# Kernel optimization log

Hardware: AMD Instinct MI355X
Metric: run time of the kernel (lower is better)

Reference implementation:

```python
import jax, jax.numpy as jnp
import numpy as np

NEG_SLOPE = 0.01  # torch LeakyReLU default
MIN_FREQ = 1.0
MAX_FREQ = 10.0
W = 100
N_HIDDEN = 100
N_OBS = 64

def _leaky(x):
    return jnp.where(x >= 0, x, NEG_SLOPE * x)

def setup_inputs() -> dict:
    key = jax.random.key(0)
    ks = jax.random.split(key, 7)
    # kaiming_uniform-ish init scales (exact init doesn't matter for correctness baseline)
    def unif(k, shape, fan_in):
        bound = np.sqrt(6.0 / fan_in)
        return jax.random.uniform(k, shape, jnp.float32, -bound, bound)
    x = jax.random.normal(ks[0], (65536, N_OBS), jnp.float32)
    W_in = unif(ks[1], (N_OBS, W), N_OBS)
    b_in = jnp.zeros((W,), jnp.float32)
    Ws = unif(ks[2], (N_HIDDEN, W, W), W)
    bs = jnp.zeros((N_HIDDEN, W), jnp.float32)
    W_out = unif(ks[3], (W, 1), W)
    b_out = jnp.zeros((1,), jnp.float32)
    return {"x": x, "W_in": W_in, "b_in": b_in, "Ws": Ws, "bs": bs,
            "W_out": W_out, "b_out": b_out}

def reference(x, W_in, b_in, Ws, bs, W_out, b_out):
    h = _leaky(x @ W_in + b_in)                       # [B, 100]
    def layer(h, wb):
        w, b = wb
        return _leaky(h @ w + b), None
    h, _ = jax.lax.scan(layer, h, (Ws, bs))           # 100 hidden layers
    a = h @ W_out + b_out                             # [B, 1]
    a = jnp.tanh(a)
    return (a + 1.0) / 2.0 * (MAX_FREQ - MIN_FREQ) + MIN_FREQ
```

## Files before the change

### kernel.cpp

```cpp
#include <hip/hip_runtime.h>
#include <cmath>

#define NLAYERS 100
#define DIN     64
#define WDIM    100
#define NPAD    112
#define NT      7
#define ROWS    32
#define PSTR    136
#define PLANE   (16 * PSTR)

typedef _Float16 half8 __attribute__((ext_vector_type(8)));
typedef __fp16   fp16x2 __attribute__((ext_vector_type(2)));
typedef float    f32x4 __attribute__((ext_vector_type(4)));

#define WSH_LAYER_HALVES (NT * 4 * 64 * 8)
#define WSH_HALVES       (NLAYERS * WSH_LAYER_HALVES)
#define W0_HALVES        (NT * 2 * 64 * 8)
#define BPAD_FLOATS      ((NLAYERS + 1) * NPAD)
#define OFF_BPAD_B       ((WSH_HALVES + W0_HALVES) * 2)
#define OFF_WOUT_B       (OFF_BPAD_B + BPAD_FLOATS * 4)
#define TOTAL_PREP       (WSH_HALVES + W0_HALVES + BPAD_FLOATS + NPAD)

__global__ void actor_prep(const float* __restrict__ Win, const float* __restrict__ bin,
                           const float* __restrict__ Ws,  const float* __restrict__ bs,
                           const float* __restrict__ Wout,
                           _Float16* __restrict__ wsh, _Float16* __restrict__ w0sh,
                           float* __restrict__ bpad, float* __restrict__ woutp) {
    int t = blockIdx.x * 256 + threadIdx.x;
    if (t < WSH_HALVES) {
        int j    = t & 7;
        int lane = (t >> 3) & 63;
        int ks   = (t >> 9) & 3;
        int rest = t >> 11;
        int nt   = rest % 7;
        int l    = rest / 7;
        int qq = lane >> 4, ll = lane & 15;
        int k = ks * 32 + qq * 8 + j;
        int n = nt * 16 + ll;
        float v = 0.f;
        if (k < WDIM && n < WDIM)       v = Ws[(l * WDIM + k) * WDIM + n];
        else if (k == 112 && n < WDIM)  v = bs[l * WDIM + n];
        wsh[t] = (_Float16)v;
        return;
    }
    int t2 = t - WSH_HALVES;
    if (t2 < W0_HALVES) {
        int j    = t2 & 7;
        int lane = (t2 >> 3) & 63;
        int ks   = (t2 >> 9) & 1;
        int nt   = t2 >> 10;
        int qq = lane >> 4, ll = lane & 15;
        int k = ks * 32 + qq * 8 + j;
        int n = nt * 16 + ll;
        float v = (k < DIN && n < WDIM) ? Win[k * WDIM + n] : 0.f;
        w0sh[t2] = (_Float16)v;
        return;
    }
    int t3 = t2 - W0_HALVES;
    if (t3 < BPAD_FLOATS) {
        int l = t3 / NPAD, c = t3 % NPAD;
        float v = 0.f;
        if (c < WDIM) v = (l == 0) ? bin[c] : bs[(l - 1) * WDIM + c];
        bpad[t3] = v;
        return;
    }
    int t4 = t3 - BPAD_FLOATS;
    if (t4 < NPAD) woutp[t4] = (t4 < WDIM) ? Wout[t4] : 0.f;
}

__device__ __forceinline__ void split8(const float* __restrict__ p, half8& hi, half8& lo) {
    f32x4 u0 = *(const f32x4*)p;
    f32x4 u1 = *(const f32x4*)(p + 4);
    float v[8] = {u0[0], u0[1], u0[2], u0[3], u1[0], u1[1], u1[2], u1[3]};
#pragma unroll
    for (int e = 0; e < 8; e += 2) {
        fp16x2 h = __builtin_amdgcn_cvt_pkrtz(v[e], v[e + 1]);
        float r0 = v[e]     - (float)h[0];
        float r1 = v[e + 1] - (float)h[1];
        fp16x2 l = __builtin_amdgcn_cvt_pkrtz(r0, r1);
        hi[e] = (_Float16)h[0]; hi[e + 1] = (_Float16)h[1];
        lo[e] = (_Float16)l[0]; lo[e + 1] = (_Float16)l[1];
    }
}

__device__ __forceinline__ void ep_tile(const f32x4 a, _Float16* __restrict__ d) {
    d[0] = (_Float16)fmaxf(a[0], 0.01f * a[0]);
    d[1] = (_Float16)fmaxf(a[1], 0.01f * a[1]);
    d[2] = (_Float16)fmaxf(a[2], 0.01f * a[2]);
    d[3] = (_Float16)fmaxf(a[3], 0.01f * a[3]);
}

__global__ __launch_bounds__(64, 2)
void actor_main(const float* __restrict__ x,
                const _Float16* __restrict__ wsh,
                const _Float16* __restrict__ w0sh,
                const float* __restrict__ bpad,
                const float* __restrict__ woutp,
                const float* __restrict__ bout,
                float* __restrict__ out) {
    __shared__ _Float16 hp[2 * PLANE];
    const int lane = threadIdx.x;
    const int q = lane >> 4, l15 = lane & 15;
    const int rowbase = blockIdx.x * ROWS;

    f32x4 acc0[NT], acc1[NT];
    half8 wb[4][NT];
    const f32x4 zero4 = {0.f, 0.f, 0.f, 0.f};

    {
        if (lane < 32) {
            const int pl = lane >> 4, row = lane & 15;
            const half8 z = {0, 0, 0, 0, 0, 0, 0, 0};
            *(half8*)(hp + pl * PLANE + row * PSTR + 112) = z;
            *(half8*)(hp + pl * PLANE + row * PSTR + 120) = z;
            hp[pl * PLANE + row * PSTR + 112] = (_Float16)1.0f;
        }
    }

#pragma unroll
    for (int ks = 0; ks < 2; ++ks)
#pragma unroll
        for (int nt = 0; nt < NT; ++nt)
            wb[ks][nt] = *(const half8*)(w0sh + ((nt * 2 + ks) * 64 + lane) * 8);
#pragma unroll
    for (int nt = 0; nt < NT; ++nt) {
        f32x4 b = *(const f32x4*)(bpad + nt * 16 + q * 4);
        acc0[nt] = b;
        acc1[nt] = b;
    }
#pragma unroll
    for (int ks = 0; ks < 2; ++ks) {
        half8 xhi, xlo;
        split8(x + (rowbase + l15) * DIN + ks * 32 + q * 8, xhi, xlo);
#pragma unroll
        for (int nt = 0; nt < NT; ++nt) {
            acc0[nt] = __builtin_amdgcn_mfma_f32_16x16x32_f16(wb[ks][nt], xhi, acc0[nt], 0, 0, 0);
            acc0[nt] = __builtin_amdgcn_mfma_f32_16x16x32_f16(wb[ks][nt], xlo, acc0[nt], 0, 0, 0);
        }
    }
#pragma unroll
    for (int ks = 0; ks < 2; ++ks) {
        half8 xhi, xlo;
        split8(x + (rowbase + 16 + l15) * DIN + ks * 32 + q * 8, xhi, xlo);
#pragma unroll
        for (int nt = 0; nt < NT; ++nt) {
            acc1[nt] = __builtin_amdgcn_mfma_f32_16x16x32_f16(wb[ks][nt], xhi, acc1[nt], 0, 0, 0);
            acc1[nt] = __builtin_amdgcn_mfma_f32_16x16x32_f16(wb[ks][nt], xlo, acc1[nt], 0, 0, 0);
        }
    }
#pragma unroll
    for (int ks = 0; ks < 4; ++ks)
#pragma unroll
        for (int nt = 0; nt < NT; ++nt)
            wb[ks][nt] = *(const half8*)(wsh + (ks * 64 + lane) * 8 + nt * 4 * 64 * 8);
#pragma unroll
    for (int nt = 0; nt < NT; ++nt)
        ep_tile(acc0[nt], hp + l15 * PSTR + nt * 16 + q * 4);

#pragma unroll 1
    for (int l = 0; l < NLAYERS; ++l) {
        const _Float16* wn = wsh + (l < NLAYERS - 1 ? l + 1 : l) * WSH_LAYER_HALVES;

        {
            f32x4 p1[NT];
#pragma unroll
            for (int nt = 0; nt < NT; ++nt) { p1[nt] = acc1[nt]; acc0[nt] = zero4; }
            _Float16* d1 = hp + PLANE + l15 * PSTR + q * 4;
#pragma unroll
            for (int ks = 0; ks < 4; ++ks) {
                half8 b0 = *(const half8*)(hp + l15 * PSTR + ks * 32 + q * 8);
#pragma unroll
                for (int nt = 0; nt < NT; ++nt)
                    acc0[nt] = __builtin_amdgcn_mfma_f32_16x16x32_f16(wb[ks][nt], b0, acc0[nt], 0, 0, 0);
                ep_tile(p1[2 * ks], d1 + (2 * ks) * 16);
                if (ks < 3) ep_tile(p1[2 * ks + 1], d1 + (2 * ks + 1) * 16);
            }
        }

        {
            f32x4 p0[NT];
#pragma unroll
            for (int nt = 0; nt < NT; ++nt) { p0[nt] = acc0[nt]; acc1[nt] = zero4; }
            _Float16* d0 = hp + l15 * PSTR + q * 4;
#pragma unroll
            for (int ks = 0; ks < 4; ++ks) {
                half8 b1 = *(const half8*)(hp + PLANE + l15 * PSTR + ks * 32 + q * 8);
#pragma unroll
                for (int nt = 0; nt < NT; ++nt)
                    acc1[nt] = __builtin_amdgcn_mfma_f32_16x16x32_f16(wb[ks][nt], b1, acc1[nt], 0, 0, 0);
#pragma unroll
                for (int nt = 0; nt < NT; ++nt)
                    wb[ks][nt] = *(const half8*)(wn + (ks * 64 + lane) * 8 + nt * 4 * 64 * 8);
                ep_tile(p0[2 * ks], d0 + (2 * ks) * 16);
                if (ks < 3) ep_tile(p0[2 * ks + 1], d0 + (2 * ks + 1) * 16);
            }
#pragma unroll
            for (int nt = 0; nt < NT; ++nt) acc0[nt] = p0[nt];
        }
    }

#pragma unroll
    for (int blk = 0; blk < 2; ++blk) {
        float s = 0.f;
#pragma unroll
        for (int nt = 0; nt < NT; ++nt) {
            f32x4 w4 = *(const f32x4*)(woutp + nt * 16 + q * 4);
            f32x4 a = blk ? acc1[nt] : acc0[nt];
#pragma unroll
            for (int r = 0; r < 4; ++r) {
                float v = fmaxf(a[r], 0.01f * a[r]);
                s += v * w4[r];
            }
        }
        s += __shfl_xor(s, 16);
        s += __shfl_xor(s, 32);
        if (q == 0) {
            float aa = s + bout[0];
            float t = tanhf(aa);
            out[rowbase + blk * 16 + l15] = t * 4.5f + 5.5f;
        }
    }
}

extern "C" void kernel_launch(void* const* d_in, const int* in_sizes, int n_in,
                              void* d_out, int out_size, void* d_ws, size_t ws_size,
                              hipStream_t stream) {
    const float* x    = (const float*)d_in[0];
    const float* Win  = (const float*)d_in[1];
    const float* bin  = (const float*)d_in[2];
    const float* Ws   = (const float*)d_in[3];
    const float* bs   = (const float*)d_in[4];
    const float* Wout = (const float*)d_in[5];
    const float* bout = (const float*)d_in[6];
    float* out = (float*)d_out;

    char* ws = (char*)d_ws;
    _Float16* wsh  = (_Float16*)ws;
    _Float16* w0sh = wsh + WSH_HALVES;
    float* bpad  = (float*)(ws + OFF_BPAD_B);
    float* woutp = (float*)(ws + OFF_WOUT_B);

    hipLaunchKernelGGL(actor_prep, dim3((TOTAL_PREP + 255) / 256), dim3(256), 0, stream,
                       Win, bin, Ws, bs, Wout, wsh, w0sh, bpad, woutp);

    const int nrows = in_sizes[0] / DIN;
    hipLaunchKernelGGL(actor_main, dim3(nrows / ROWS), dim3(64), 0, stream,
                       x, wsh, w0sh, bpad, woutp, bout, out);
}
```

Baseline: 286.9 us.

## Reorder weight fragment layout by ks, pack fp16 epilogue, drop accumulator copies

Reorders the prepacked weight fragments so the 7 n-tiles of one k-slice sit contiguously, which makes each per-ks prefetch a single contiguous 7KB chunk. The LeakyReLU epilogue now converts to fp16 first and does packed half2 max and multiply, storing 8 bytes at once instead of four scalar half stores. The p0/p1 accumulator copies are removed, which cuts register pressure and move instructions. Applying the activation in fp16 instead of fp32 changes rounding slightly.

```diff
diff --git a/kernel.cpp b/kernel.cpp
--- a/kernel.cpp
+++ b/kernel.cpp
@@ -11,12 +11,13 @@
 #define PLANE   (16 * PSTR)
 
 typedef _Float16 half8 __attribute__((ext_vector_type(8)));
+typedef _Float16 half2v __attribute__((ext_vector_type(2)));
 typedef __fp16   fp16x2 __attribute__((ext_vector_type(2)));
 typedef float    f32x4 __attribute__((ext_vector_type(4)));
 
-#define WSH_LAYER_HALVES (NT * 4 * 64 * 8)
+#define WSH_LAYER_HALVES (4 * NT * 64 * 8)
 #define WSH_HALVES       (NLAYERS * WSH_LAYER_HALVES)
-#define W0_HALVES        (NT * 2 * 64 * 8)
+#define W0_HALVES        (2 * NT * 64 * 8)
 #define BPAD_FLOATS      ((NLAYERS + 1) * NPAD)
 #define OFF_BPAD_B       ((WSH_HALVES + W0_HALVES) * 2)
 #define OFF_WOUT_B       (OFF_BPAD_B + BPAD_FLOATS * 4)
@@ -31,10 +32,11 @@
     if (t < WSH_HALVES) {
         int j    = t & 7;
         int lane = (t >> 3) & 63;
-        int ks   = (t >> 9) & 3;
-        int rest = t >> 11;
-        int nt   = rest % 7;
-        int l    = rest / 7;
+        int fid  = t >> 9;
+        int nt   = fid % 7;
+        int r2   = fid / 7;
+        int ks   = r2 & 3;
+        int l    = r2 >> 2;
         int qq = lane >> 4, ll = lane & 15;
         int k = ks * 32 + qq * 8 + j;
         int n = nt * 16 + ll;
@@ -48,8 +50,9 @@
     if (t2 < W0_HALVES) {
         int j    = t2 & 7;
         int lane = (t2 >> 3) & 63;
-        int ks   = (t2 >> 9) & 1;
-        int nt   = t2 >> 10;
+        int fid  = t2 >> 9;
+        int nt   = fid % 7;
+        int ks   = fid / 7;
         int qq = lane >> 4, ll = lane & 15;
         int k = ks * 32 + qq * 8 + j;
         int n = nt * 16 + ll;
@@ -85,10 +88,16 @@
 }
 
 __device__ __forceinline__ void ep_tile(const f32x4 a, _Float16* __restrict__ d) {
-    d[0] = (_Float16)fmaxf(a[0], 0.01f * a[0]);
-    d[1] = (_Float16)fmaxf(a[1], 0.01f * a[1]);
-    d[2] = (_Float16)fmaxf(a[2], 0.01f * a[2]);
-    d[3] = (_Float16)fmaxf(a[3], 0.01f * a[3]);
+    half2v p01, p23;
+    p01[0] = (_Float16)a[0]; p01[1] = (_Float16)a[1];
+    p23[0] = (_Float16)a[2]; p23[1] = (_Float16)a[3];
+    const half2v slope = {(_Float16)0.01f, (_Float16)0.01f};
+    p01 = __builtin_elementwise_max(p01, p01 * slope);
+    p23 = __builtin_elementwise_max(p23, p23 * slope);
+    uint2 w;
+    w.x = __builtin_bit_cast(unsigned, p01);
+    w.y = __builtin_bit_cast(unsigned, p23);
+    *reinterpret_cast<uint2*>(d) = w;
 }
 
 __global__ __launch_bounds__(64, 2)
@@ -122,7 +131,7 @@
     for (int ks = 0; ks < 2; ++ks)
 #pragma unroll
         for (int nt = 0; nt < NT; ++nt)
-            wb[ks][nt] = *(const half8*)(w0sh + ((nt * 2 + ks) * 64 + lane) * 8);
+            wb[ks][nt] = *(const half8*)(w0sh + (ks * 7 + nt) * 512 + lane * 8);
 #pragma unroll
     for (int nt = 0; nt < NT; ++nt) {
         f32x4 b = *(const f32x4*)(bpad + nt * 16 + q * 4);
@@ -150,10 +159,12 @@
         }
     }
 #pragma unroll
-    for (int ks = 0; ks < 4; ++ks)
+    for (int ks = 0; ks < 4; ++ks) {
+        const _Float16* wk = wsh + (ks * 7) * 512;
 #pragma unroll
         for (int nt = 0; nt < NT; ++nt)
-            wb[ks][nt] = *(const half8*)(wsh + (ks * 64 + lane) * 8 + nt * 4 * 64 * 8);
+            wb[ks][nt] = *(const half8*)(wk + nt * 512 + lane * 8);
+    }
 #pragma unroll
     for (int nt = 0; nt < NT; ++nt)
         ep_tile(acc0[nt], hp + l15 * PSTR + nt * 16 + q * 4);
@@ -163,9 +174,8 @@
         const _Float16* wn = wsh + (l < NLAYERS - 1 ? l + 1 : l) * WSH_LAYER_HALVES;
 
         {
-            f32x4 p1[NT];
-#pragma unroll
-            for (int nt = 0; nt < NT; ++nt) { p1[nt] = acc1[nt]; acc0[nt] = zero4; }
+#pragma unroll
+            for (int nt = 0; nt < NT; ++nt) acc0[nt] = zero4;
             _Float16* d1 = hp + PLANE + l15 * PSTR + q * 4;
 #pragma unroll
             for (int ks = 0; ks < 4; ++ks) {
@@ -173,15 +183,14 @@
 #pragma unroll
                 for (int nt = 0; nt < NT; ++nt)
                     acc0[nt] = __builtin_amdgcn_mfma_f32_16x16x32_f16(wb[ks][nt], b0, acc0[nt], 0, 0, 0);
-                ep_tile(p1[2 * ks], d1 + (2 * ks) * 16);
-                if (ks < 3) ep_tile(p1[2 * ks + 1], d1 + (2 * ks + 1) * 16);
+                ep_tile(acc1[2 * ks], d1 + (2 * ks) * 16);
+                if (ks < 3) ep_tile(acc1[2 * ks + 1], d1 + (2 * ks + 1) * 16);
             }
         }
 
         {
-            f32x4 p0[NT];
-#pragma unroll
-            for (int nt = 0; nt < NT; ++nt) { p0[nt] = acc0[nt]; acc1[nt] = zero4; }
+#pragma unroll
+            for (int nt = 0; nt < NT; ++nt) acc1[nt] = zero4;
             _Float16* d0 = hp + l15 * PSTR + q * 4;
 #pragma unroll
             for (int ks = 0; ks < 4; ++ks) {
@@ -189,14 +198,13 @@
 #pragma unroll
                 for (int nt = 0; nt < NT; ++nt)
                     acc1[nt] = __builtin_amdgcn_mfma_f32_16x16x32_f16(wb[ks][nt], b1, acc1[nt], 0, 0, 0);
+                const _Float16* wk = wn + (ks * 7) * 512;
 #pragma unroll
                 for (int nt = 0; nt < NT; ++nt)
-                    wb[ks][nt] = *(const half8*)(wn + (ks * 64 + lane) * 8 + nt * 4 * 64 * 8);
-                ep_tile(p0[2 * ks], d0 + (2 * ks) * 16);
-                if (ks < 3) ep_tile(p0[2 * ks + 1], d0 + (2 * ks + 1) * 16);
+                    wb[ks][nt] = *(const half8*)(wk + nt * 512 + lane * 8);
+                ep_tile(acc0[2 * ks], d0 + (2 * ks) * 16);
+                if (ks < 3) ep_tile(acc0[2 * ks + 1], d0 + (2 * ks + 1) * 16);
             }
-#pragma unroll
-            for (int nt = 0; nt < NT; ++nt) acc0[nt] = p0[nt];
         }
     }
 
```

Measured after the change: 271.8 us. 1.06x faster.
